# Kernel tuning notes

Hardware: AMD Instinct MI355X
Metric: run time of the kernel (lower is better)

## Reference

```python
import jax, jax.numpy as jnp
import numpy as np

K = 7  # kernel_size


def setup_inputs() -> dict:
    key = jax.random.key(0)
    ks = jax.random.split(key, 7)
    B, C, H, W = 32, 256, 56, 56
    x = jax.random.normal(ks[0], (B, C, H, W), jnp.float32)
    # BatchNorm2d affine params
    bn_gamma = 1.0 + 0.1 * jax.random.normal(ks[1], (C,), jnp.float32)
    bn_beta = 0.1 * jax.random.normal(ks[2], (C,), jnp.float32)
    # Linear(k^2 -> k), torch weight layout (out, in)
    w0 = jax.random.normal(ks[3], (K, K * K), jnp.float32) / np.sqrt(K * K)
    # LayerNorm([C, k]) affine params
    ln_gamma = 1.0 + 0.1 * jax.random.normal(ks[4], (C, K), jnp.float32)
    ln_beta = 0.1 * jax.random.normal(ks[5], (C, K), jnp.float32)
    # Linear(k -> k^2)
    w1 = jax.random.normal(ks[6], (K * K, K), jnp.float32) / np.sqrt(K)
    return dict(x=x, bn_gamma=bn_gamma, bn_beta=bn_beta, w0=w0,
                ln_gamma=ln_gamma, ln_beta=ln_beta, w1=w1)


def reference(x, bn_gamma, bn_beta, w0, ln_gamma, ln_beta, w1):
    B, C, H, W = x.shape
    k = K
    eps = 1e-5
    # AdaptiveAvgPool2d((k,k)); H,W divisible by k -> exact block means
    p = x.reshape(B, C, k, H // k, k, W // k).mean(axis=(3, 5))  # (B,C,k,k)
    # BatchNorm2d (training-mode batch statistics, biased variance)
    mu = p.mean(axis=(0, 2, 3), keepdims=True)
    var = p.var(axis=(0, 2, 3), keepdims=True)
    p = (p - mu) * jax.lax.rsqrt(var + eps)
    p = p * bn_gamma[None, :, None, None] + bn_beta[None, :, None, None]
    # b c kh kw -> b c (kh kw), then Linear(k^2 -> k)
    v = p.reshape(B, C, k * k) @ w0.T  # (B,C,k)
    # LayerNorm over the (C,k) normalized shape
    m = v.mean(axis=(1, 2), keepdims=True)
    s = v.var(axis=(1, 2), keepdims=True)
    v = (v - m) * jax.lax.rsqrt(s + eps) * ln_gamma[None] + ln_beta[None]
    v = jax.nn.sigmoid(v)
    v = v @ w1.T  # (B,C,k^2)
    kern = v.reshape(B * C, 1, k, k)  # per-sample, per-channel depthwise kernels
    # F.conv2d(groups=B*C, padding='same', stride=1); odd k -> 'SAME' matches torch
    out = jax.lax.conv_general_dilated(
        x.reshape(1, B * C, H, W), kern,
        window_strides=(1, 1), padding='SAME',
        feature_group_count=B * C,
        dimension_numbers=('NCHW', 'OIHW', 'NCHW'))
    return out.reshape(B, C, H, W)
```

## Files before the change

### kernel.cpp

```cpp
#include <hip/hip_runtime.h>
#include <math.h>

#define BATCH 32
#define CH    256
#define HH    56
#define WW    56
#define HW    3136
#define KS    7
#define KK    49
#define NIMG  8192
#define CPITCH 72
#define CROWS  62
#define CPIMG  (CROWS*CPITCH)
#define CIPB   2

__global__ __launch_bounds__(256) void pool_kernel(const float* __restrict__ x,
                                                   float* __restrict__ p,
                                                   float2* __restrict__ ss) {
    const int t  = threadIdx.x;
    const int im = t >> 7, tl = t & 127;
    const int img = blockIdx.x * 2 + im;
    const bool active = tl < 98;
    float s = 0.f;
    if (active) {
        const int cq = tl % 14, pr = tl / 14;
        const float4* xr = (const float4*)(x + (size_t)img * HW);
        #pragma unroll
        for (int r = 0; r < 8; ++r) {
            const float4 v = xr[(pr * 8 + r) * 14 + cq];
            s += (v.x + v.y) + (v.z + v.w);
        }
    }
    const float cellv = (s + __shfl_xor(s, 1, 64)) * (1.0f / 64.0f);
    float v = 0.f;
    if (active && !(tl & 1)) {
        const int cq = tl % 14, pr = tl / 14;
        p[(size_t)img * KK + pr * KS + (cq >> 1)] = cellv;
        v = cellv;
    }
    float v2 = v * v;
    #pragma unroll
    for (int o = 32; o >= 1; o >>= 1) {
        v  += __shfl_down(v,  o, 64);
        v2 += __shfl_down(v2, o, 64);
    }
    __shared__ float ps1[4], ps2[4];
    if ((t & 63) == 0) { ps1[t >> 6] = v; ps2[t >> 6] = v2; }
    __syncthreads();
    if (t == 0)  ss[img]     = make_float2(ps1[0] + ps1[1], ps2[0] + ps2[1]);
    if (t == 64) ss[img + 1] = make_float2(ps1[2] + ps1[3], ps2[2] + ps2[3]);
}

__global__ __launch_bounds__(256) void mid_kernel(const float* __restrict__ p,
                                                  const float2* __restrict__ ss,
                                                  const float* __restrict__ bng,
                                                  const float* __restrict__ bnb,
                                                  const float* __restrict__ w0,
                                                  const float* __restrict__ lng,
                                                  const float* __restrict__ lnb,
                                                  const float* __restrict__ w1,
                                                  float* __restrict__ ker) {
    const int b = blockIdx.x, c = threadIdx.x;
    __shared__ float s_w0[KS * KK], s_w1[KK * KS];
    __shared__ float r1[4], r2[4];
    for (int i = c; i < KS * KK; i += 256) { s_w0[i] = w0[i]; s_w1[i] = w1[i]; }
    float S = 0.f, S2 = 0.f;
    #pragma unroll 4
    for (int bb = 0; bb < BATCH; ++bb) {
        const float2 t2 = ss[(size_t)bb * CH + c];
        S += t2.x; S2 += t2.y;
    }
    {
        const float inv  = 1.0f / (float)(BATCH * KK);
        const float mu   = S * inv;
        const float var  = S2 * inv - mu * mu;
        const float rstd = rsqrtf(var + 1e-5f);
        S  = bng[c] * rstd;
        S2 = bnb[c] - mu * S;
    }
    __syncthreads();
    float pn[KK];
    const float* pp = p + ((size_t)b * CH + c) * KK;
    #pragma unroll
    for (int i = 0; i < KK; ++i) pn[i] = pp[i] * S + S2;
    float v[KS];
    float ls = 0.f, ls2 = 0.f;
    #pragma unroll
    for (int j = 0; j < KS; ++j) {
        float a = 0.f;
        #pragma unroll
        for (int i = 0; i < KK; ++i) a += pn[i] * s_w0[j * KK + i];
        v[j] = a; ls += a; ls2 += a * a;
    }
    #pragma unroll
    for (int o = 32; o >= 1; o >>= 1) {
        ls  += __shfl_down(ls, o, 64);
        ls2 += __shfl_down(ls2, o, 64);
    }
    const int w = threadIdx.x >> 6;
    if ((threadIdx.x & 63) == 0) { r1[w] = ls; r2[w] = ls2; }
    __syncthreads();
    const float Sv  = r1[0] + r1[1] + r1[2] + r1[3];
    const float Sv2 = r2[0] + r2[1] + r2[2] + r2[3];
    const float inv = 1.0f / (float)(CH * KS);
    const float m   = Sv * inv;
    const float var = Sv2 * inv - m * m;
    const float rs  = rsqrtf(var + 1e-5f);
    float sg[KS];
    #pragma unroll
    for (int j = 0; j < KS; ++j) {
        const float vn = (v[j] - m) * rs * lng[c * KS + j] + lnb[c * KS + j];
        sg[j] = 1.0f / (1.0f + expf(-vn));
    }
    float* ko = ker + ((size_t)b * CH + c) * KK;
    #pragma unroll
    for (int i = 0; i < KK; ++i) {
        float a = 0.f;
        #pragma unroll
        for (int j = 0; j < KS; ++j) a += sg[j] * s_w1[i * KS + j];
        ko[i] = a;
    }
}

__global__ __launch_bounds__(256) void conv_kernel(const float* __restrict__ x,
                                                   const float* __restrict__ ker,
                                                   float* __restrict__ out) {
    __shared__ __align__(16) float pad[CIPB * CPIMG];
    __shared__ float kfl[CIPB * KK];
    const int t    = threadIdx.x;
    const int img0 = blockIdx.x * CIPB;
    if (t < CIPB * KK) kfl[t] = ker[(size_t)img0 * KK + t];
    float4* pz = (float4*)pad;
    for (int j = t; j < CIPB * CPIMG / 4; j += 256)
        pz[j] = make_float4(0.f, 0.f, 0.f, 0.f);
    __syncthreads();
    for (int jj = t; jj < CIPB * 784; jj += 256) {
        const int imS = (jj >= 784) ? 1 : 0;
        const int j   = jj - imS * 784;
        const int r   = j / 14, c4 = j - r * 14;
        const float4 v = *(const float4*)(x + (size_t)(img0 + imS) * HW + r * WW + c4 * 4);
        float* d = pad + imS * CPIMG + (r + 3) * CPITCH + c4 * 4 + 3;
        d[0] = v.x; d[1] = v.y; d[2] = v.z; d[3] = v.w;
    }
    __syncthreads();
    const int im = t >> 7, tl = t & 127;
    const int q = tl & 15, st = tl >> 4;
    const int oc0 = q * 4, orow0 = st * 7;
    float kv[KK];
    #pragma unroll
    for (int i = 0; i < KK; ++i)
        kv[i] = __int_as_float(__builtin_amdgcn_readfirstlane(__float_as_int(kfl[im * KK + i])));
    const float* pb = pad + im * CPIMG + orow0 * CPITCH + oc0;
    float acc[KS][4];
    #pragma unroll
    for (int a = 0; a < KS; ++a)
        #pragma unroll
        for (int d = 0; d < 4; ++d) acc[a][d] = 0.f;
    #pragma unroll
    for (int ri = 0; ri < 13; ++ri) {
        const float4 A  = *(const float4*)(pb + ri * CPITCH);
        const float4 Bv = *(const float4*)(pb + ri * CPITCH + 4);
        const float4 Cv = *(const float4*)(pb + ri * CPITCH + 8);
        const float w[12] = {A.x, A.y, A.z, A.w, Bv.x, Bv.y, Bv.z, Bv.w,
                             Cv.x, Cv.y, Cv.z, Cv.w};
        #pragma unroll
        for (int kr = 0; kr < KS; ++kr) {
            const int orow = ri - kr;
            if (orow < 0 || orow > 6) continue;
            #pragma unroll
            for (int kw = 0; kw < KS; ++kw) {
                const float kvv = kv[kr * KS + kw];
                acc[orow][0] += w[kw    ] * kvv;
                acc[orow][1] += w[kw + 1] * kvv;
                acc[orow][2] += w[kw + 2] * kvv;
                acc[orow][3] += w[kw + 3] * kvv;
            }
        }
    }
    if (q < 14) {
        float* oi = out + (size_t)(img0 + im) * HW;
        #pragma unroll
        for (int rr = 0; rr < KS; ++rr)
            *(float4*)&oi[(orow0 + rr) * WW + oc0] =
                make_float4(acc[rr][0], acc[rr][1], acc[rr][2], acc[rr][3]);
    }
}

extern "C" void kernel_launch(void* const* d_in, const int* in_sizes, int n_in,
                              void* d_out, int out_size, void* d_ws, size_t ws_size,
                              hipStream_t stream) {
    const float* x   = (const float*)d_in[0];
    const float* bng = (const float*)d_in[1];
    const float* bnb = (const float*)d_in[2];
    const float* w0  = (const float*)d_in[3];
    const float* lng = (const float*)d_in[4];
    const float* lnb = (const float*)d_in[5];
    const float* w1  = (const float*)d_in[6];
    float* out = (float*)d_out;

    float* ws   = (float*)d_ws;
    float* p    = ws;
    float* kern = p + (size_t)NIMG * KK;
    float2* ss  = (float2*)d_out;

    hipLaunchKernelGGL(pool_kernel, dim3(NIMG / 2),    dim3(256), 0, stream, x, p, ss);
    hipLaunchKernelGGL(mid_kernel,  dim3(BATCH),       dim3(256), 0, stream, p, ss,
                       bng, bnb, w0, lng, lnb, w1, kern);
    hipLaunchKernelGGL(conv_kernel, dim3(NIMG / CIPB), dim3(256), 0, stream, x, kern, out);
}
```

Before: 249.6 us.

## Restructure pool and conv kernels to one image per wave-group with per-wave tiles

The pool kernel now gives each wave one image, accumulates the 7x7 cell sums with LDS atomics and writes per-image stats directly, with no block-level barrier. The conv kernel now processes one image per block. Each wave stages a 20-row padded tile with scalar loads and computes 14 output rows per lane, one output column per lane, replacing the 2-image block with 4x7 register tiles and float4 reads. The aim is to drop block-wide syncs and the whole-image zero fill and to raise occupancy. In exchange it adds halo overfetch (20 rows per 14), scalar global and LDS accesses, and 8 idle lanes per wave.

Result: slower. 262.0 us (+5.0%).

```diff
diff --git a/kernel.cpp b/kernel.cpp
--- a/kernel.cpp
+++ b/kernel.cpp
@@ -9,34 +9,37 @@
 #define KS    7
 #define KK    49
 #define NIMG  8192
-#define CPITCH 72
-#define CROWS  62
-#define CPIMG  (CROWS*CPITCH)
-#define CIPB   2
+#define TPITCH 62
+#define TROWS  20
+#define TSIZE  (TPITCH * TROWS)
 
 __global__ __launch_bounds__(256) void pool_kernel(const float* __restrict__ x,
                                                    float* __restrict__ p,
                                                    float2* __restrict__ ss) {
-    const int t  = threadIdx.x;
-    const int im = t >> 7, tl = t & 127;
-    const int img = blockIdx.x * 2 + im;
-    const bool active = tl < 98;
-    float s = 0.f;
-    if (active) {
-        const int cq = tl % 14, pr = tl / 14;
-        const float4* xr = (const float4*)(x + (size_t)img * HW);
-        #pragma unroll
-        for (int r = 0; r < 8; ++r) {
-            const float4 v = xr[(pr * 8 + r) * 14 + cq];
-            s += (v.x + v.y) + (v.z + v.w);
+    __shared__ float cells[4][KK];
+    const int t = threadIdx.x;
+    const int wid = t >> 6, lane = t & 63;
+    const int img = blockIdx.x * 4 + wid;
+    float* cw = cells[wid];
+    if (lane < KK) cw[lane] = 0.f;
+    asm volatile("s_waitcnt lgkmcnt(0)" ::: "memory");
+    __builtin_amdgcn_wave_barrier();
+    const float4* xp = (const float4*)(x + (size_t)img * HW);
+    #pragma unroll
+    for (int k = 0; k < 13; ++k) {
+        const int j = k * 64 + lane;
+        if (j < 784) {
+            const float4 v = xp[j];
+            const int r = j / 14, q = j - r * 14;
+            atomicAdd(&cw[(r >> 3) * KS + (q >> 1)], (v.x + v.y) + (v.z + v.w));
         }
     }
-    const float cellv = (s + __shfl_xor(s, 1, 64)) * (1.0f / 64.0f);
+    asm volatile("s_waitcnt lgkmcnt(0)" ::: "memory");
+    __builtin_amdgcn_wave_barrier();
     float v = 0.f;
-    if (active && !(tl & 1)) {
-        const int cq = tl % 14, pr = tl / 14;
-        p[(size_t)img * KK + pr * KS + (cq >> 1)] = cellv;
-        v = cellv;
+    if (lane < KK) {
+        v = cw[lane] * (1.0f / 64.0f);
+        p[(size_t)img * KK + lane] = v;
     }
     float v2 = v * v;
     #pragma unroll
@@ -44,11 +47,7 @@
         v  += __shfl_down(v,  o, 64);
         v2 += __shfl_down(v2, o, 64);
     }
-    __shared__ float ps1[4], ps2[4];
-    if ((t & 63) == 0) { ps1[t >> 6] = v; ps2[t >> 6] = v2; }
-    __syncthreads();
-    if (t == 0)  ss[img]     = make_float2(ps1[0] + ps1[1], ps2[0] + ps2[1]);
-    if (t == 64) ss[img + 1] = make_float2(ps1[2] + ps1[3], ps2[2] + ps2[3]);
+    if (lane == 0) ss[img] = make_float2(v, v2);
 }
 
 __global__ __launch_bounds__(256) void mid_kernel(const float* __restrict__ p,
@@ -122,67 +121,58 @@
     }
 }
 
-__global__ __launch_bounds__(256) void conv_kernel(const float* __restrict__ x,
-                                                   const float* __restrict__ ker,
-                                                   float* __restrict__ out) {
-    __shared__ __align__(16) float pad[CIPB * CPIMG];
-    __shared__ float kfl[CIPB * KK];
-    const int t    = threadIdx.x;
-    const int img0 = blockIdx.x * CIPB;
-    if (t < CIPB * KK) kfl[t] = ker[(size_t)img0 * KK + t];
-    float4* pz = (float4*)pad;
-    for (int j = t; j < CIPB * CPIMG / 4; j += 256)
-        pz[j] = make_float4(0.f, 0.f, 0.f, 0.f);
-    __syncthreads();
-    for (int jj = t; jj < CIPB * 784; jj += 256) {
-        const int imS = (jj >= 784) ? 1 : 0;
-        const int j   = jj - imS * 784;
-        const int r   = j / 14, c4 = j - r * 14;
-        const float4 v = *(const float4*)(x + (size_t)(img0 + imS) * HW + r * WW + c4 * 4);
-        float* d = pad + imS * CPIMG + (r + 3) * CPITCH + c4 * 4 + 3;
-        d[0] = v.x; d[1] = v.y; d[2] = v.z; d[3] = v.w;
-    }
-    __syncthreads();
-    const int im = t >> 7, tl = t & 127;
-    const int q = tl & 15, st = tl >> 4;
-    const int oc0 = q * 4, orow0 = st * 7;
-    float kv[KK];
+__global__ __launch_bounds__(256, 6) void conv_kernel(const float* __restrict__ x,
+                                                      const float* __restrict__ ker,
+                                                      float* __restrict__ out) {
+    __shared__ float tile[4 * TSIZE];
+    const int t = threadIdx.x;
+    const int wid = t >> 6, lane = t & 63;
+    const int img = blockIdx.x;
+    const int r0 = wid * 14;
+    float* tl = tile + wid * TSIZE;
+    const float* kp = ker + (size_t)img * KK;
+    float tap[KK];
     #pragma unroll
     for (int i = 0; i < KK; ++i)
-        kv[i] = __int_as_float(__builtin_amdgcn_readfirstlane(__float_as_int(kfl[im * KK + i])));
-    const float* pb = pad + im * CPIMG + orow0 * CPITCH + oc0;
-    float acc[KS][4];
-    #pragma unroll
-    for (int a = 0; a < KS; ++a)
-        #pragma unroll
-        for (int d = 0; d < 4; ++d) acc[a][d] = 0.f;
-    #pragma unroll
-    for (int ri = 0; ri < 13; ++ri) {
-        const float4 A  = *(const float4*)(pb + ri * CPITCH);
-        const float4 Bv = *(const float4*)(pb + ri * CPITCH + 4);
-        const float4 Cv = *(const float4*)(pb + ri * CPITCH + 8);
-        const float w[12] = {A.x, A.y, A.z, A.w, Bv.x, Bv.y, Bv.z, Bv.w,
-                             Cv.x, Cv.y, Cv.z, Cv.w};
+        tap[i] = __int_as_float(__builtin_amdgcn_readfirstlane(__float_as_int(kp[i])));
+    const float* xi = x + (size_t)img * HW;
+    #pragma unroll
+    for (int rr = 0; rr < TROWS; ++rr) {
+        const int g = r0 + rr - 3;
+        if (lane < 56) {
+            float v = 0.f;
+            if ((unsigned)g < 56u) v = xi[g * WW + lane];
+            tl[rr * TPITCH + lane + 3] = v;
+        } else {
+            const int j = lane - 56;
+            if (j < 6) tl[rr * TPITCH + ((j < 3) ? j : 56 + j)] = 0.f;
+        }
+    }
+    asm volatile("s_waitcnt lgkmcnt(0)" ::: "memory");
+    __builtin_amdgcn_wave_barrier();
+    const int cc = (lane < 56) ? lane : 55;
+    float acc[14];
+    #pragma unroll
+    for (int o = 0; o < 14; ++o) acc[o] = 0.f;
+    #pragma unroll
+    for (int rr = 0; rr < TROWS; ++rr) {
+        float w[KS];
+        #pragma unroll
+        for (int kw = 0; kw < KS; ++kw) w[kw] = tl[rr * TPITCH + cc + kw];
         #pragma unroll
         for (int kr = 0; kr < KS; ++kr) {
-            const int orow = ri - kr;
-            if (orow < 0 || orow > 6) continue;
+            const int o = rr - kr;
+            if (o < 0 || o > 13) continue;
             #pragma unroll
-            for (int kw = 0; kw < KS; ++kw) {
-                const float kvv = kv[kr * KS + kw];
-                acc[orow][0] += w[kw    ] * kvv;
-                acc[orow][1] += w[kw + 1] * kvv;
-                acc[orow][2] += w[kw + 2] * kvv;
-                acc[orow][3] += w[kw + 3] * kvv;
-            }
+            for (int kw = 0; kw < KS; ++kw)
+                acc[o] += w[kw] * tap[kr * KS + kw];
         }
     }
-    if (q < 14) {
-        float* oi = out + (size_t)(img0 + im) * HW;
-        #pragma unroll
-        for (int rr = 0; rr < KS; ++rr)
-            *(float4*)&oi[(orow0 + rr) * WW + oc0] =
-                make_float4(acc[rr][0], acc[rr][1], acc[rr][2], acc[rr][3]);
+    if (lane < 56) {
+        float* oi = out + (size_t)img * HW;
+        #pragma unroll
+        for (int o = 0; o < 14; ++o)
+            oi[(r0 + o) * WW + lane] = acc[o];
     }
 }
 
@@ -203,8 +193,8 @@
     float* kern = p + (size_t)NIMG * KK;
     float2* ss  = (float2*)d_out;
 
-    hipLaunchKernelGGL(pool_kernel, dim3(NIMG / 2),    dim3(256), 0, stream, x, p, ss);
-    hipLaunchKernelGGL(mid_kernel,  dim3(BATCH),       dim3(256), 0, stream, p, ss,
+    hipLaunchKernelGGL(pool_kernel, dim3(NIMG / 4), dim3(256), 0, stream, x, p, ss);
+    hipLaunchKernelGGL(mid_kernel,  dim3(BATCH),    dim3(256), 0, stream, p, ss,
                        bng, bnb, w0, lng, lnb, w1, kern);
-    hipLaunchKernelGGL(conv_kernel, dim3(NIMG / CIPB), dim3(256), 0, stream, x, kern, out);
-}
+    hipLaunchKernelGGL(conv_kernel, dim3(NIMG),     dim3(256), 0, stream, x, kern, out);
+}
```
